# Optimization experiments

Measured on AMD Instinct MI355X. Metric: run time of the kernel, lower is better.

The kernel has to match this reference:

```python
import jax, jax.numpy as jnp
import numpy as np

D = 512        # embed_dim
H = 2048       # expert hidden (4*D)
E = 8          # num_experts
TOPK = 2       # num_experts_per_tok


def setup_inputs() -> dict:
    key = jax.random.key(0)
    ks = jax.random.split(key, 5)
    s = 0.02
    x = jax.random.normal(ks[0], (4, 8192, D), dtype=jnp.float32)
    gate_w = jax.random.normal(ks[1], (D, E), dtype=jnp.float32) * s
    W1 = jax.random.normal(ks[2], (E, D, H), dtype=jnp.float32) * s
    W3 = jax.random.normal(ks[3], (E, D, H), dtype=jnp.float32) * s
    W2 = jax.random.normal(ks[4], (E, H, D), dtype=jnp.float32) * s
    return {"x": x, "gate_w": gate_w, "W1": W1, "W2": W2, "W3": W3}


def reference(x, gate_w, W1, W2, W3):
    B, S, _ = x.shape
    xt = x.reshape(-1, D)                      # [T, D]
    T = xt.shape[0]
    gate_logits = xt @ gate_w                  # [T, E]
    w, idx = jax.lax.top_k(gate_logits, TOPK)  # [T, k]
    w = jax.nn.softmax(w, axis=1).astype(xt.dtype)
    # combine weights: comb[t, e] = routing weight of expert e for token t (0 if unselected)
    comb = jnp.zeros((T, E), dtype=xt.dtype).at[jnp.arange(T)[:, None], idx].add(w)
    out = jnp.zeros_like(xt)
    for e in range(E):
        h = jax.nn.silu(xt @ W1[e]) * (xt @ W3[e])   # [T, H]
        out = out + (h @ W2[e]) * comb[:, e:e + 1]
    return out.reshape(B, S, D)
```

## Files before the change

kernel.cpp:

```cpp
#include <hip/hip_runtime.h>
#include <stdint.h>

#define D_DIM 512
#define H_DIM 2048
#define E_NUM 8
#define TOPK_N 2

typedef __attribute__((ext_vector_type(8))) short bf16x8;
typedef __attribute__((ext_vector_type(4))) float f32x4;

#define GLOAD_LDS16(gsrc, ldst)                                                     \
    __builtin_amdgcn_global_load_lds(                                               \
        (const __attribute__((address_space(1))) void*)(gsrc),                      \
        (__attribute__((address_space(3))) void*)(ldst), 16, 0, 0)

static __device__ __forceinline__ unsigned short f2bf(float f) {
    unsigned u = __float_as_uint(f);
    unsigned r = (u + 0x7fffu + ((u >> 16) & 1u)) >> 16;
    return (unsigned short)r;
}

__global__ void init_kernel(int* list_token, float* list_w, unsigned short* zrow, int cap) {
    int id = blockIdx.x * blockDim.x + threadIdx.x;
    if (id < cap) { list_token[id] = -1; list_w[id] = 0.f; }
    if (id < D_DIM) zrow[id] = 0;
}

__global__ void gwt_kernel(const float* __restrict__ gw, float* __restrict__ gwT) {
    int id = blockIdx.x * blockDim.x + threadIdx.x;
    int e = id >> 9, d = id & 511;
    gwT[id] = gw[d * E_NUM + e];
}

__global__ void gate_cvt_kernel(const float* __restrict__ x, const float* __restrict__ gwT,
                                unsigned short* __restrict__ xb,
                                int* __restrict__ ridx, float* __restrict__ rw, int T) {
    int wave = threadIdx.x >> 6;
    int lane = threadIdx.x & 63;
    int t = blockIdx.x * 4 + wave;
    if (t >= T) return;
    const float* xr = x + (size_t)t * D_DIM + lane * 8;
    float4 a = *(const float4*)xr;
    float4 b = *(const float4*)(xr + 4);
    union { unsigned short s[8]; uint4 v; } o;
    o.s[0] = f2bf(a.x); o.s[1] = f2bf(a.y); o.s[2] = f2bf(a.z); o.s[3] = f2bf(a.w);
    o.s[4] = f2bf(b.x); o.s[5] = f2bf(b.y); o.s[6] = f2bf(b.z); o.s[7] = f2bf(b.w);
    *(uint4*)(xb + (size_t)t * D_DIM + lane * 8) = o.v;
    float acc[8];
#pragma unroll
    for (int e = 0; e < 8; ++e) {
        const float* g = gwT + e * D_DIM + lane * 8;
        float4 g0 = *(const float4*)g;
        float4 g1 = *(const float4*)(g + 4);
        acc[e] = a.x * g0.x + a.y * g0.y + a.z * g0.z + a.w * g0.w
               + b.x * g1.x + b.y * g1.y + b.z * g1.z + b.w * g1.w;
    }
#pragma unroll
    for (int off = 32; off > 0; off >>= 1) {
#pragma unroll
        for (int e = 0; e < 8; ++e) acc[e] += __shfl_xor(acc[e], off, 64);
    }
    if (lane == 0) {
        int e0 = 0; float l0 = acc[0];
#pragma unroll
        for (int e = 1; e < 8; ++e) if (acc[e] > l0) { l0 = acc[e]; e0 = e; }
        int e1 = -1; float l1 = -1e30f;
#pragma unroll
        for (int e = 0; e < 8; ++e) if (e != e0 && acc[e] > l1) { l1 = acc[e]; e1 = e; }
        float w0 = 1.f / (1.f + expf(l1 - l0));
        ridx[t * 2] = e0; ridx[t * 2 + 1] = e1;
        rw[t * 2] = w0;  rw[t * 2 + 1] = 1.f - w0;
    }
}

__global__ void tconv_kernel(const float* __restrict__ in, unsigned short* __restrict__ out,
                             int R, int C) {
    __shared__ float tile[32][33];
    int e = blockIdx.z;
    const float* src = in + (size_t)e * R * C;
    unsigned short* dst = out + (size_t)e * R * C;
    int c = blockIdx.x * 32 + threadIdx.x;
#pragma unroll
    for (int i = 0; i < 4; ++i) {
        int r = blockIdx.y * 32 + threadIdx.y + i * 8;
        tile[threadIdx.y + i * 8][threadIdx.x] = src[(size_t)r * C + c];
    }
    __syncthreads();
    int r2 = blockIdx.y * 32 + threadIdx.x;
#pragma unroll
    for (int i = 0; i < 4; ++i) {
        int c2 = blockIdx.x * 32 + threadIdx.y + i * 8;
        dst[(size_t)c2 * R + r2] = f2bf(tile[threadIdx.x][threadIdx.y + i * 8]);
    }
}

__global__ void hist_kernel(const int* __restrict__ ridx, int* __restrict__ partial, int npairs) {
    __shared__ int cnt[E_NUM];
    if (threadIdx.x < E_NUM) cnt[threadIdx.x] = 0;
    __syncthreads();
    for (int i = blockIdx.x * blockDim.x + threadIdx.x; i < npairs; i += gridDim.x * blockDim.x)
        atomicAdd(&cnt[ridx[i]], 1);
    __syncthreads();
    if (threadIdx.x < E_NUM) partial[blockIdx.x * E_NUM + threadIdx.x] = cnt[threadIdx.x];
}

__global__ void scan_kernel(const int* __restrict__ partial, int* __restrict__ seg,
                            int* __restrict__ block_base) {
    __shared__ int sp[64 * E_NUM];
    __shared__ int segl[E_NUM + 1];
    int tid = threadIdx.x;
    if (tid < 64 * E_NUM) sp[tid] = partial[tid];
    __syncthreads();
    if (tid == 0) {
        int off = 0;
        for (int e = 0; e < E_NUM; ++e) {
            segl[e] = off;
            int c = 0;
            for (int b = 0; b < 64; ++b) c += sp[b * E_NUM + e];
            off += (c + 127) & ~127;
        }
        segl[E_NUM] = off;
    }
    __syncthreads();
    if (tid < E_NUM) {
        int run = segl[tid];
        for (int b = 0; b < 64; ++b) { block_base[b * E_NUM + tid] = run; run += sp[b * E_NUM + tid]; }
        seg[tid] = segl[tid];
        if (tid == 0) seg[E_NUM] = segl[E_NUM];
    }
}

__global__ void scatter_kernel(const int* __restrict__ ridx, const float* __restrict__ rw,
                               const int* __restrict__ block_base,
                               int* __restrict__ list_token, float* __restrict__ list_w, int npairs) {
    __shared__ int base[E_NUM];
    __shared__ int cnt[E_NUM];
    if (threadIdx.x < E_NUM) { base[threadIdx.x] = block_base[blockIdx.x * E_NUM + threadIdx.x]; cnt[threadIdx.x] = 0; }
    __syncthreads();
    for (int i = blockIdx.x * blockDim.x + threadIdx.x; i < npairs; i += gridDim.x * blockDim.x) {
        int e = ridx[i];
        int pos = base[e] + atomicAdd(&cnt[e], 1);
        list_token[pos] = i >> 1;
        list_w[pos] = rw[i];
    }
}

__global__ __launch_bounds__(256) void gemm1_kernel(
    const unsigned short* __restrict__ xb,
    const unsigned short* __restrict__ w1t,
    const unsigned short* __restrict__ w3t,
    const unsigned short* __restrict__ zrow,
    const int* __restrict__ list_token,
    const int* __restrict__ seg,
    unsigned short* __restrict__ hbuf,
    int chunk_base, int MT, int MG) {
    __shared__ short As[2][128 * 64];
    __shared__ short Bs[2][128 * 64];

    int bfl = blockIdx.x;
    int xcd = bfl & 7;
    int idx = bfl >> 3;
    int mlocal = idx % MG;
    int yt = idx / MG;
    int mt = mlocal * 8 + xcd;
    if (mt >= MT) return;

    int tid = threadIdx.x;
    int w = tid >> 6, l = tid & 63;
    int m0 = mt * 128;
    int slot0 = chunk_base + m0;
    int n0 = yt * 64;

    int e = 0;
#pragma unroll
    for (int i = 0; i < E_NUM - 1; ++i) if (slot0 >= seg[i + 1]) e = i + 1;
    const unsigned short* b1 = w1t + ((size_t)e * H_DIM + n0) * D_DIM;
    const unsigned short* b3 = w3t + ((size_t)e * H_DIM + n0) * D_DIM;

    int lr8 = l >> 3, p = l & 7;
    const unsigned short* aptr[4];
    const unsigned short* bptr[4];
#pragma unroll
    for (int q = 0; q < 4; ++q) {
        int row = (q * 4 + w) * 8 + lr8;
        int c = p ^ (row & 7);
        int tok = list_token[slot0 + row];
        aptr[q] = (tok >= 0 ? xb + (size_t)tok * D_DIM : zrow) + c * 8;
        bptr[q] = (row < 64 ? b1 + (size_t)row * D_DIM
                            : b3 + (size_t)(row - 64) * D_DIM) + c * 8;
    }

    int wm = (w & 1) * 64;
    int wn = (w >> 1) * 32;
    int lrr = l & 15;
    int lk = (l >> 4) * 8;

    f32x4 acc1[4][2] = {};
    f32x4 acc3[4][2] = {};

#define G1_STAGE(K0, BUF)                                                           \
    {                                                                               \
        _Pragma("unroll")                                                           \
        for (int q = 0; q < 4; ++q) {                                               \
            GLOAD_LDS16(aptr[q] + (K0), &As[BUF][(q * 4 + w) * 512]);               \
            GLOAD_LDS16(bptr[q] + (K0), &Bs[BUF][(q * 4 + w) * 512]);               \
        }                                                                           \
    }

#define G1_COMPUTE(BUF)                                                             \
    {                                                                               \
        _Pragma("unroll")                                                           \
        for (int ks = 0; ks < 64; ks += 32) {                                       \
            int cblk = (ks + lk) >> 3;                                              \
            bf16x8 af[4], b1f[2], b3f[2];                                           \
            _Pragma("unroll")                                                       \
            for (int i = 0; i < 4; ++i) {                                           \
                int row = wm + i * 16 + lrr;                                        \
                af[i] = *(const bf16x8*)&As[BUF][row * 64 + ((cblk ^ (row & 7)) << 3)]; \
            }                                                                       \
            _Pragma("unroll")                                                       \
            for (int j = 0; j < 2; ++j) {                                           \
                int r1 = wn + j * 16 + lrr;                                         \
                b1f[j] = *(const bf16x8*)&Bs[BUF][r1 * 64 + ((cblk ^ (r1 & 7)) << 3)]; \
                int r3 = 64 + wn + j * 16 + lrr;                                    \
                b3f[j] = *(const bf16x8*)&Bs[BUF][r3 * 64 + ((cblk ^ (r3 & 7)) << 3)]; \
            }                                                                       \
            __builtin_amdgcn_s_setprio(1);                                          \
            _Pragma("unroll")                                                       \
            for (int i = 0; i < 4; ++i)                                             \
                _Pragma("unroll")                                                   \
                for (int j = 0; j < 2; ++j) {                                       \
                    acc1[i][j] = __builtin_amdgcn_mfma_f32_16x16x32_bf16(af[i], b1f[j], acc1[i][j], 0, 0, 0); \
                    acc3[i][j] = __builtin_amdgcn_mfma_f32_16x16x32_bf16(af[i], b3f[j], acc3[i][j], 0, 0, 0); \
                }                                                                   \
            __builtin_amdgcn_s_setprio(0);                                          \
        }                                                                           \
    }

    G1_STAGE(0, 0);
    __syncthreads();
#pragma unroll
    for (int t = 0; t < 8; t += 2) {
        G1_STAGE((t + 1) * 64, 1);
        G1_COMPUTE(0);
        __syncthreads();
        if (t + 2 < 8) G1_STAGE((t + 2) * 64, 0);
        G1_COMPUTE(1);
        __syncthreads();
    }
#undef G1_STAGE
#undef G1_COMPUTE

    int lrow0 = (l >> 4) * 4, lcol = l & 15;
#pragma unroll
    for (int i = 0; i < 4; ++i)
#pragma unroll
        for (int j = 0; j < 2; ++j)
#pragma unroll
            for (int r = 0; r < 4; ++r) {
                int row = wm + i * 16 + lrow0 + r;
                int col = wn + j * 16 + lcol;
                float v1 = acc1[i][j][r];
                float v3 = acc3[i][j][r];
                float h = v1 / (1.f + __expf(-v1)) * v3;
                hbuf[(size_t)(m0 + row) * H_DIM + n0 + col] = f2bf(h);
            }
}

__global__ __launch_bounds__(256) void gemm2_kernel(
    const unsigned short* __restrict__ hbuf,
    const unsigned short* __restrict__ w2t,
    const int* __restrict__ list_token,
    const float* __restrict__ list_w,
    const int* __restrict__ seg,
    float* __restrict__ out,
    int chunk_base, int MT) {
    __shared__ short As[2][128 * 64];
    __shared__ short Bs[2][128 * 64];

    int bfl = blockIdx.x;
    int xcd = bfl & 7;
    int idx = bfl >> 3;
    int yt = idx & 3;
    int mlocal = idx >> 2;
    int mt = mlocal * 8 + xcd;
    if (mt >= MT) return;

    int tid = threadIdx.x;
    int w = tid >> 6, l = tid & 63;
    int m0 = mt * 128;
    int slot0 = chunk_base + m0;
    int n0 = yt * 128;

    int e = 0;
#pragma unroll
    for (int i = 0; i < E_NUM - 1; ++i) if (slot0 >= seg[i + 1]) e = i + 1;
    const unsigned short* b2 = w2t + ((size_t)e * D_DIM + n0) * H_DIM;

    int lr8 = l >> 3, p = l & 7;
    const unsigned short* aptr[4];
    const unsigned short* bptr[4];
#pragma unroll
    for (int q = 0; q < 4; ++q) {
        int row = (q * 4 + w) * 8 + lr8;
        int c = p ^ (row & 7);
        aptr[q] = hbuf + (size_t)(m0 + row) * H_DIM + c * 8;
        bptr[q] = b2 + (size_t)row * H_DIM + c * 8;
    }

    int wm = (w & 1) * 64;
    int wn = (w >> 1) * 64;
    int lrr = l & 15;
    int lk = (l >> 4) * 8;

    f32x4 acc[4][4] = {};

#define G2_STAGE(K0, BUF)                                                           \
    {                                                                               \
        _Pragma("unroll")                                                           \
        for (int q = 0; q < 4; ++q) {                                               \
            GLOAD_LDS16(aptr[q] + (K0), &As[BUF][(q * 4 + w) * 512]);               \
            GLOAD_LDS16(bptr[q] + (K0), &Bs[BUF][(q * 4 + w) * 512]);               \
        }                                                                           \
    }

#define G2_COMPUTE(BUF)                                                             \
    {                                                                               \
        _Pragma("unroll")                                                           \
        for (int ks = 0; ks < 64; ks += 32) {                                       \
            int cblk = (ks + lk) >> 3;                                              \
            bf16x8 af[4], bf[4];                                                    \
            _Pragma("unroll")                                                       \
            for (int i = 0; i < 4; ++i) {                                           \
                int row = wm + i * 16 + lrr;                                        \
                af[i] = *(const bf16x8*)&As[BUF][row * 64 + ((cblk ^ (row & 7)) << 3)]; \
            }                                                                       \
            _Pragma("unroll")                                                       \
            for (int j = 0; j < 4; ++j) {                                           \
                int row = wn + j * 16 + lrr;                                        \
                bf[j] = *(const bf16x8*)&Bs[BUF][row * 64 + ((cblk ^ (row & 7)) << 3)]; \
            }                                                                       \
            __builtin_amdgcn_s_setprio(1);                                          \
            _Pragma("unroll")                                                       \
            for (int i = 0; i < 4; ++i)                                             \
                _Pragma("unroll")                                                   \
                for (int j = 0; j < 4; ++j)                                         \
                    acc[i][j] = __builtin_amdgcn_mfma_f32_16x16x32_bf16(af[i], bf[j], acc[i][j], 0, 0, 0); \
            __builtin_amdgcn_s_setprio(0);                                          \
        }                                                                           \
    }

    G2_STAGE(0, 0);
    __syncthreads();
    for (int t = 0; t < 32; t += 2) {
        G2_STAGE((t + 1) * 64, 1);
        G2_COMPUTE(0);
        __syncthreads();
        if (t + 2 < 32) G2_STAGE((t + 2) * 64, 0);
        G2_COMPUTE(1);
        __syncthreads();
    }
#undef G2_STAGE
#undef G2_COMPUTE

    int lrow0 = (l >> 4) * 4, lcol = l & 15;
#pragma unroll
    for (int i = 0; i < 4; ++i)
#pragma unroll
        for (int r = 0; r < 4; ++r) {
            int row = wm + i * 16 + lrow0 + r;
            int tok = list_token[slot0 + row];
            if (tok < 0) continue;
            float wgt = list_w[slot0 + row];
#pragma unroll
            for (int j = 0; j < 4; ++j) {
                int col = wn + j * 16 + lcol;
                atomicAdd(&out[(size_t)tok * D_DIM + n0 + col], acc[i][j][r] * wgt);
            }
        }
}

extern "C" void kernel_launch(void* const* d_in, const int* in_sizes, int n_in,
                              void* d_out, int out_size, void* d_ws, size_t ws_size,
                              hipStream_t stream) {
    const float* x  = (const float*)d_in[0];
    const float* gw = (const float*)d_in[1];
    const float* W1 = (const float*)d_in[2];
    const float* W2 = (const float*)d_in[3];
    const float* W3 = (const float*)d_in[4];
    float* out = (float*)d_out;

    int T = in_sizes[0] / D_DIM;
    int npairs = T * TOPK_N;
    const int CAP = npairs + E_NUM * 128;

    char* p = (char*)d_ws;
    size_t off = 0;
    auto take = [&](size_t bytes) {
        char* r = p + off;
        off = (off + bytes + 255) & ~(size_t)255;
        return r;
    };
    int* seg           = (int*)take((E_NUM + 1) * 4);
    int* partial       = (int*)take(64 * E_NUM * 4);
    int* block_base    = (int*)take(64 * E_NUM * 4);
    int* list_token    = (int*)take((size_t)CAP * 4);
    float* list_w      = (float*)take((size_t)CAP * 4);
    int* ridx          = (int*)take((size_t)npairs * 4);
    float* rw          = (float*)take((size_t)npairs * 4);
    float* gwT         = (float*)take((size_t)E_NUM * D_DIM * 4);
    unsigned short* zrow = (unsigned short*)take((size_t)D_DIM * 2);
    unsigned short* xb  = (unsigned short*)take((size_t)T * D_DIM * 2);
    unsigned short* w1t = (unsigned short*)take((size_t)E_NUM * D_DIM * H_DIM * 2);
    unsigned short* w3t = (unsigned short*)take((size_t)E_NUM * D_DIM * H_DIM * 2);
    unsigned short* w2t = (unsigned short*)take((size_t)E_NUM * D_DIM * H_DIM * 2);

    size_t hbuf2_bytes = (size_t)(CAP / 2) * H_DIM * 2;
    int NCHUNK = (ws_size >= off + hbuf2_bytes + 4096) ? 2 : 4;
    int chunk_slots = CAP / NCHUNK;
    int MT = chunk_slots / 128;
    int MG = (MT + 7) / 8;
    unsigned short* hbuf = (unsigned short*)take((size_t)chunk_slots * H_DIM * 2);

    hipMemsetAsync(d_out, 0, (size_t)out_size * sizeof(float), stream);

    init_kernel<<<(CAP + 255) / 256, 256, 0, stream>>>(list_token, list_w, zrow, CAP);
    gwt_kernel<<<(E_NUM * D_DIM) / 256, 256, 0, stream>>>(gw, gwT);

    gate_cvt_kernel<<<T / 4, 256, 0, stream>>>(x, gwT, xb, ridx, rw, T);

    dim3 tb(32, 8);
    tconv_kernel<<<dim3(H_DIM / 32, D_DIM / 32, E_NUM), tb, 0, stream>>>(W1, w1t, D_DIM, H_DIM);
    tconv_kernel<<<dim3(H_DIM / 32, D_DIM / 32, E_NUM), tb, 0, stream>>>(W3, w3t, D_DIM, H_DIM);
    tconv_kernel<<<dim3(D_DIM / 32, H_DIM / 32, E_NUM), tb, 0, stream>>>(W2, w2t, H_DIM, D_DIM);

    hist_kernel<<<64, 256, 0, stream>>>(ridx, partial, npairs);
    scan_kernel<<<1, 512, 0, stream>>>(partial, seg, block_base);
    scatter_kernel<<<64, 256, 0, stream>>>(ridx, rw, block_base, list_token, list_w, npairs);

    int g1_grid = 8 * MG * (H_DIM / 64);
    int g2_grid = 8 * MG * (D_DIM / 128);
    for (int c = 0; c < NCHUNK; ++c) {
        int cb = c * chunk_slots;
        gemm1_kernel<<<g1_grid, 256, 0, stream>>>(
            xb, w1t, w3t, zrow, list_token, seg, hbuf, cb, MT, MG);
        gemm2_kernel<<<g2_grid, 256, 0, stream>>>(
            hbuf, w2t, list_token, list_w, seg, out, cb, MT);
    }
}
```

Measured before the change: 917.0 us.

## Deepen GEMM prefetch with vmcnt waits and force four hidden-buffer chunks

```diff
diff --git a/kernel.cpp b/kernel.cpp
--- a/kernel.cpp
+++ b/kernel.cpp
@@ -13,6 +13,10 @@
     __builtin_amdgcn_global_load_lds(                                               \
         (const __attribute__((address_space(1))) void*)(gsrc),                      \
         (__attribute__((address_space(3))) void*)(ldst), 16, 0, 0)
+
+#define WAITVM(N) asm volatile("s_waitcnt vmcnt(" #N ")" ::: "memory")
+#define SCB() __builtin_amdgcn_sched_barrier(0)
+#define BAR() __builtin_amdgcn_s_barrier()
 
 static __device__ __forceinline__ unsigned short f2bf(float f) {
     unsigned u = __float_as_uint(f);
@@ -238,15 +242,23 @@
     }
 
     G1_STAGE(0, 0);
-    __syncthreads();
+    G1_STAGE(64, 1);
 #pragma unroll
     for (int t = 0; t < 8; t += 2) {
-        G1_STAGE((t + 1) * 64, 1);
+        WAITVM(8);
+        BAR();
+        SCB();
         G1_COMPUTE(0);
-        __syncthreads();
+        SCB();
+        BAR();
         if (t + 2 < 8) G1_STAGE((t + 2) * 64, 0);
+        if (t < 6) { WAITVM(8); } else { WAITVM(0); }
+        BAR();
+        SCB();
         G1_COMPUTE(1);
-        __syncthreads();
+        SCB();
+        BAR();
+        if (t + 3 < 8) G1_STAGE((t + 3) * 64, 1);
     }
 #undef G1_STAGE
 #undef G1_COMPUTE
@@ -351,15 +363,35 @@
     }
 
     G2_STAGE(0, 0);
-    __syncthreads();
-    for (int t = 0; t < 32; t += 2) {
-        G2_STAGE((t + 1) * 64, 1);
+    G2_STAGE(64, 1);
+    for (int t = 0; t < 30; t += 2) {
+        WAITVM(8);
+        BAR();
+        SCB();
         G2_COMPUTE(0);
-        __syncthreads();
-        if (t + 2 < 32) G2_STAGE((t + 2) * 64, 0);
+        SCB();
+        BAR();
+        G2_STAGE((t + 2) * 64, 0);
+        WAITVM(8);
+        BAR();
+        SCB();
         G2_COMPUTE(1);
-        __syncthreads();
-    }
+        SCB();
+        BAR();
+        G2_STAGE((t + 3) * 64, 1);
+    }
+    WAITVM(8);
+    BAR();
+    SCB();
+    G2_COMPUTE(0);
+    SCB();
+    BAR();
+    WAITVM(0);
+    BAR();
+    SCB();
+    G2_COMPUTE(1);
+    SCB();
+    BAR();
 #undef G2_STAGE
 #undef G2_COMPUTE
 
@@ -393,6 +425,10 @@
     int T = in_sizes[0] / D_DIM;
     int npairs = T * TOPK_N;
     const int CAP = npairs + E_NUM * 128;
+    const int NCHUNK = 4;
+    int chunk_slots = CAP / NCHUNK;
+    int MT = chunk_slots / 128;
+    int MG = (MT + 7) / 8;
 
     char* p = (char*)d_ws;
     size_t off = 0;
@@ -414,13 +450,8 @@
     unsigned short* w1t = (unsigned short*)take((size_t)E_NUM * D_DIM * H_DIM * 2);
     unsigned short* w3t = (unsigned short*)take((size_t)E_NUM * D_DIM * H_DIM * 2);
     unsigned short* w2t = (unsigned short*)take((size_t)E_NUM * D_DIM * H_DIM * 2);
-
-    size_t hbuf2_bytes = (size_t)(CAP / 2) * H_DIM * 2;
-    int NCHUNK = (ws_size >= off + hbuf2_bytes + 4096) ? 2 : 4;
-    int chunk_slots = CAP / NCHUNK;
-    int MT = chunk_slots / 128;
-    int MG = (MT + 7) / 8;
     unsigned short* hbuf = (unsigned short*)take((size_t)chunk_slots * H_DIM * 2);
+    (void)ws_size;
 
     hipMemsetAsync(d_out, 0, (size_t)out_size * sizeof(float), stream);
 
```

Measured after the change: 956.0 us. 1.04x slower.

## Use 4-stage K=32 LDS pipeline with vmcnt waits in both expert GEMMs

Applied to the files above, without the earlier changes.

```diff
diff --git a/kernel.cpp b/kernel.cpp
--- a/kernel.cpp
+++ b/kernel.cpp
@@ -13,6 +13,10 @@
     __builtin_amdgcn_global_load_lds(                                               \
         (const __attribute__((address_space(1))) void*)(gsrc),                      \
         (__attribute__((address_space(3))) void*)(ldst), 16, 0, 0)
+
+#define WAITVM(N) asm volatile("s_waitcnt vmcnt(" #N ")" ::: "memory")
+#define SCB() __builtin_amdgcn_sched_barrier(0)
+#define BAR() __builtin_amdgcn_s_barrier()
 
 static __device__ __forceinline__ unsigned short f2bf(float f) {
     unsigned u = __float_as_uint(f);
@@ -154,8 +158,8 @@
     const int* __restrict__ seg,
     unsigned short* __restrict__ hbuf,
     int chunk_base, int MT, int MG) {
-    __shared__ short As[2][128 * 64];
-    __shared__ short Bs[2][128 * 64];
+    __shared__ __align__(16) short As[4][4096];
+    __shared__ __align__(16) short Bs[4][4096];
 
     int bfl = blockIdx.x;
     int xcd = bfl & 7;
@@ -177,79 +181,95 @@
     const unsigned short* b1 = w1t + ((size_t)e * H_DIM + n0) * D_DIM;
     const unsigned short* b3 = w3t + ((size_t)e * H_DIM + n0) * D_DIM;
 
-    int lr8 = l >> 3, p = l & 7;
-    const unsigned short* aptr[4];
-    const unsigned short* bptr[4];
-#pragma unroll
-    for (int q = 0; q < 4; ++q) {
-        int row = (q * 4 + w) * 8 + lr8;
-        int c = p ^ (row & 7);
-        int tok = list_token[slot0 + row];
-        aptr[q] = (tok >= 0 ? xb + (size_t)tok * D_DIM : zrow) + c * 8;
-        bptr[q] = (row < 64 ? b1 + (size_t)row * D_DIM
-                            : b3 + (size_t)(row - 64) * D_DIM) + c * 8;
-    }
+    int seg0 = w, seg1 = 4 + w;
+    int r0 = seg0 * 16 + (l >> 2);
+    int r1 = seg1 * 16 + (l >> 2);
+    int gsrc8 = ((l & 3) ^ ((l >> 3) & 3)) * 8;
+    int tok0 = list_token[slot0 + r0];
+    int tok1 = list_token[slot0 + r1];
+    const unsigned short* pa0 = (tok0 >= 0 ? xb + (size_t)tok0 * D_DIM : zrow) + gsrc8;
+    const unsigned short* pa1 = (tok1 >= 0 ? xb + (size_t)tok1 * D_DIM : zrow) + gsrc8;
+    const unsigned short* pb0 = b1 + (size_t)r0 * D_DIM + gsrc8;
+    const unsigned short* pb1 = b3 + (size_t)(r1 - 64) * D_DIM + gsrc8;
 
     int wm = (w & 1) * 64;
     int wn = (w >> 1) * 32;
     int lrr = l & 15;
-    int lk = (l >> 4) * 8;
+    int gq = l >> 4;
+    int aoff[4], b1o[2], b3o[2];
+#pragma unroll
+    for (int i = 0; i < 4; ++i) {
+        int row = wm + i * 16 + lrr;
+        aoff[i] = row * 64 + ((gq ^ ((row >> 1) & 3)) << 4);
+    }
+#pragma unroll
+    for (int j = 0; j < 2; ++j) {
+        int rA = wn + j * 16 + lrr;
+        b1o[j] = rA * 64 + ((gq ^ ((rA >> 1) & 3)) << 4);
+        int rB = 64 + wn + j * 16 + lrr;
+        b3o[j] = rB * 64 + ((gq ^ ((rB >> 1) & 3)) << 4);
+    }
 
     f32x4 acc1[4][2] = {};
     f32x4 acc3[4][2] = {};
 
-#define G1_STAGE(K0, BUF)                                                           \
+#define G1_STAGE(KO, SBUF)                                                          \
     {                                                                               \
-        _Pragma("unroll")                                                           \
-        for (int q = 0; q < 4; ++q) {                                               \
-            GLOAD_LDS16(aptr[q] + (K0), &As[BUF][(q * 4 + w) * 512]);               \
-            GLOAD_LDS16(bptr[q] + (K0), &Bs[BUF][(q * 4 + w) * 512]);               \
-        }                                                                           \
+        GLOAD_LDS16(pa0 + (KO) * 32, &As[SBUF][seg0 * 512]);                        \
+        GLOAD_LDS16(pa1 + (KO) * 32, &As[SBUF][seg1 * 512]);                        \
+        GLOAD_LDS16(pb0 + (KO) * 32, &Bs[SBUF][seg0 * 512]);                        \
+        GLOAD_LDS16(pb1 + (KO) * 32, &Bs[SBUF][seg1 * 512]);                        \
     }
 
 #define G1_COMPUTE(BUF)                                                             \
     {                                                                               \
+        const char* Ab = (const char*)As[BUF];                                      \
+        const char* Bb = (const char*)Bs[BUF];                                      \
+        bf16x8 af[4], f1[2], f3[2];                                                 \
         _Pragma("unroll")                                                           \
-        for (int ks = 0; ks < 64; ks += 32) {                                       \
-            int cblk = (ks + lk) >> 3;                                              \
-            bf16x8 af[4], b1f[2], b3f[2];                                           \
-            _Pragma("unroll")                                                       \
-            for (int i = 0; i < 4; ++i) {                                           \
-                int row = wm + i * 16 + lrr;                                        \
-                af[i] = *(const bf16x8*)&As[BUF][row * 64 + ((cblk ^ (row & 7)) << 3)]; \
-            }                                                                       \
+        for (int i = 0; i < 4; ++i) af[i] = *(const bf16x8*)(Ab + aoff[i]);         \
+        _Pragma("unroll")                                                           \
+        for (int j = 0; j < 2; ++j) {                                               \
+            f1[j] = *(const bf16x8*)(Bb + b1o[j]);                                  \
+            f3[j] = *(const bf16x8*)(Bb + b3o[j]);                                  \
+        }                                                                           \
+        __builtin_amdgcn_s_setprio(1);                                              \
+        _Pragma("unroll")                                                           \
+        for (int i = 0; i < 4; ++i)                                                 \
             _Pragma("unroll")                                                       \
             for (int j = 0; j < 2; ++j) {                                           \
-                int r1 = wn + j * 16 + lrr;                                         \
-                b1f[j] = *(const bf16x8*)&Bs[BUF][r1 * 64 + ((cblk ^ (r1 & 7)) << 3)]; \
-                int r3 = 64 + wn + j * 16 + lrr;                                    \
-                b3f[j] = *(const bf16x8*)&Bs[BUF][r3 * 64 + ((cblk ^ (r3 & 7)) << 3)]; \
+                acc1[i][j] = __builtin_amdgcn_mfma_f32_16x16x32_bf16(af[i], f1[j], acc1[i][j], 0, 0, 0); \
+                acc3[i][j] = __builtin_amdgcn_mfma_f32_16x16x32_bf16(af[i], f3[j], acc3[i][j], 0, 0, 0); \
             }                                                                       \
-            __builtin_amdgcn_s_setprio(1);                                          \
-            _Pragma("unroll")                                                       \
-            for (int i = 0; i < 4; ++i)                                             \
-                _Pragma("unroll")                                                   \
-                for (int j = 0; j < 2; ++j) {                                       \
-                    acc1[i][j] = __builtin_amdgcn_mfma_f32_16x16x32_bf16(af[i], b1f[j], acc1[i][j], 0, 0, 0); \
-                    acc3[i][j] = __builtin_amdgcn_mfma_f32_16x16x32_bf16(af[i], b3f[j], acc3[i][j], 0, 0, 0); \
-                }                                                                   \
-            __builtin_amdgcn_s_setprio(0);                                          \
-        }                                                                           \
-    }
+        __builtin_amdgcn_s_setprio(0);                                              \
+    }
+
+#define G1_STEP8S(T, CB, SB) { WAITVM(8); BAR(); SCB(); G1_STAGE((T) + 3, SB); G1_COMPUTE(CB); }
+#define G1_STEP8(CB)  { WAITVM(8); BAR(); SCB(); G1_COMPUTE(CB); }
+#define G1_STEP4(CB)  { WAITVM(4); BAR(); SCB(); G1_COMPUTE(CB); }
+#define G1_STEP0(CB)  { WAITVM(0); BAR(); SCB(); G1_COMPUTE(CB); }
 
     G1_STAGE(0, 0);
-    __syncthreads();
-#pragma unroll
-    for (int t = 0; t < 8; t += 2) {
-        G1_STAGE((t + 1) * 64, 1);
-        G1_COMPUTE(0);
-        __syncthreads();
-        if (t + 2 < 8) G1_STAGE((t + 2) * 64, 0);
-        G1_COMPUTE(1);
-        __syncthreads();
-    }
+    G1_STAGE(1, 1);
+    G1_STAGE(2, 2);
+#pragma unroll
+    for (int t = 0; t < 12; t += 4) {
+        G1_STEP8S(t + 0, 0, 3);
+        G1_STEP8S(t + 1, 1, 0);
+        G1_STEP8S(t + 2, 2, 1);
+        G1_STEP8S(t + 3, 3, 2);
+    }
+    G1_STEP8S(12, 0, 3);
+    G1_STEP8(1);
+    G1_STEP4(2);
+    G1_STEP0(3);
+
 #undef G1_STAGE
 #undef G1_COMPUTE
+#undef G1_STEP8S
+#undef G1_STEP8
+#undef G1_STEP4
+#undef G1_STEP0
 
     int lrow0 = (l >> 4) * 4, lcol = l & 15;
 #pragma unroll
@@ -275,8 +295,8 @@
     const int* __restrict__ seg,
     float* __restrict__ out,
     int chunk_base, int MT) {
-    __shared__ short As[2][128 * 64];
-    __shared__ short Bs[2][128 * 64];
+    __shared__ __align__(16) short As[4][4096];
+    __shared__ __align__(16) short Bs[4][4096];
 
     int bfl = blockIdx.x;
     int xcd = bfl & 7;
@@ -297,71 +317,82 @@
     for (int i = 0; i < E_NUM - 1; ++i) if (slot0 >= seg[i + 1]) e = i + 1;
     const unsigned short* b2 = w2t + ((size_t)e * D_DIM + n0) * H_DIM;
 
-    int lr8 = l >> 3, p = l & 7;
-    const unsigned short* aptr[4];
-    const unsigned short* bptr[4];
-#pragma unroll
-    for (int q = 0; q < 4; ++q) {
-        int row = (q * 4 + w) * 8 + lr8;
-        int c = p ^ (row & 7);
-        aptr[q] = hbuf + (size_t)(m0 + row) * H_DIM + c * 8;
-        bptr[q] = b2 + (size_t)row * H_DIM + c * 8;
-    }
+    int seg0 = w, seg1 = 4 + w;
+    int r0 = seg0 * 16 + (l >> 2);
+    int r1 = seg1 * 16 + (l >> 2);
+    int gsrc8 = ((l & 3) ^ ((l >> 3) & 3)) * 8;
+    const unsigned short* pa0 = hbuf + (size_t)(m0 + r0) * H_DIM + gsrc8;
+    const unsigned short* pa1 = hbuf + (size_t)(m0 + r1) * H_DIM + gsrc8;
+    const unsigned short* pb0 = b2 + (size_t)r0 * H_DIM + gsrc8;
+    const unsigned short* pb1 = b2 + (size_t)r1 * H_DIM + gsrc8;
 
     int wm = (w & 1) * 64;
     int wn = (w >> 1) * 64;
     int lrr = l & 15;
-    int lk = (l >> 4) * 8;
+    int gq = l >> 4;
+    int aoff[4], boff[4];
+#pragma unroll
+    for (int i = 0; i < 4; ++i) {
+        int rowA = wm + i * 16 + lrr;
+        aoff[i] = rowA * 64 + ((gq ^ ((rowA >> 1) & 3)) << 4);
+        int rowB = wn + i * 16 + lrr;
+        boff[i] = rowB * 64 + ((gq ^ ((rowB >> 1) & 3)) << 4);
+    }
 
     f32x4 acc[4][4] = {};
 
-#define G2_STAGE(K0, BUF)                                                           \
+#define G2_STAGE(KO, SBUF)                                                          \
     {                                                                               \
-        _Pragma("unroll")                                                           \
-        for (int q = 0; q < 4; ++q) {                                               \
-            GLOAD_LDS16(aptr[q] + (K0), &As[BUF][(q * 4 + w) * 512]);               \
-            GLOAD_LDS16(bptr[q] + (K0), &Bs[BUF][(q * 4 + w) * 512]);               \
-        }                                                                           \
+        GLOAD_LDS16(pa0 + (KO) * 32, &As[SBUF][seg0 * 512]);                        \
+        GLOAD_LDS16(pa1 + (KO) * 32, &As[SBUF][seg1 * 512]);                        \
+        GLOAD_LDS16(pb0 + (KO) * 32, &Bs[SBUF][seg0 * 512]);                        \
+        GLOAD_LDS16(pb1 + (KO) * 32, &Bs[SBUF][seg1 * 512]);                        \
     }
 
 #define G2_COMPUTE(BUF)                                                             \
     {                                                                               \
+        const char* Ab = (const char*)As[BUF];                                      \
+        const char* Bb = (const char*)Bs[BUF];                                      \
+        bf16x8 af[4], bf[4];                                                        \
         _Pragma("unroll")                                                           \
-        for (int ks = 0; ks < 64; ks += 32) {                                       \
-            int cblk = (ks + lk) >> 3;                                              \
-            bf16x8 af[4], bf[4];                                                    \
+        for (int i = 0; i < 4; ++i) {                                               \
+            af[i] = *(const bf16x8*)(Ab + aoff[i]);                                 \
+            bf[i] = *(const bf16x8*)(Bb + boff[i]);                                 \
+        }                                                                           \
+        __builtin_amdgcn_s_setprio(1);                                              \
+        _Pragma("unroll")                                                           \
+        for (int i = 0; i < 4; ++i)                                                 \
             _Pragma("unroll")                                                       \
-            for (int i = 0; i < 4; ++i) {                                           \
-                int row = wm + i * 16 + lrr;                                        \
-                af[i] = *(const bf16x8*)&As[BUF][row * 64 + ((cblk ^ (row & 7)) << 3)]; \
-            }                                                                       \
-            _Pragma("unroll")                                                       \
-            for (int j = 0; j < 4; ++j) {                                           \
-                int row = wn + j * 16 + lrr;                                        \
-                bf[j] = *(const bf16x8*)&Bs[BUF][row * 64 + ((cblk ^ (row & 7)) << 3)]; \
-            }                                                                       \
-            __builtin_amdgcn_s_setprio(1);                                          \
-            _Pragma("unroll")                                                       \
-            for (int i = 0; i < 4; ++i)                                             \
-                _Pragma("unroll")                                                   \
-                for (int j = 0; j < 4; ++j)                                         \
-                    acc[i][j] = __builtin_amdgcn_mfma_f32_16x16x32_bf16(af[i], bf[j], acc[i][j], 0, 0, 0); \
-            __builtin_amdgcn_s_setprio(0);                                          \
-        }                                                                           \
-    }
+            for (int j = 0; j < 4; ++j)                                             \
+                acc[i][j] = __builtin_amdgcn_mfma_f32_16x16x32_bf16(af[i], bf[j], acc[i][j], 0, 0, 0); \
+        __builtin_amdgcn_s_setprio(0);                                              \
+    }
+
+#define G2_STEP8S(T, CB, SB) { WAITVM(8); BAR(); SCB(); G2_STAGE((T) + 3, SB); G2_COMPUTE(CB); }
+#define G2_STEP8(CB)  { WAITVM(8); BAR(); SCB(); G2_COMPUTE(CB); }
+#define G2_STEP4(CB)  { WAITVM(4); BAR(); SCB(); G2_COMPUTE(CB); }
+#define G2_STEP0(CB)  { WAITVM(0); BAR(); SCB(); G2_COMPUTE(CB); }
 
     G2_STAGE(0, 0);
-    __syncthreads();
-    for (int t = 0; t < 32; t += 2) {
-        G2_STAGE((t + 1) * 64, 1);
-        G2_COMPUTE(0);
-        __syncthreads();
-        if (t + 2 < 32) G2_STAGE((t + 2) * 64, 0);
-        G2_COMPUTE(1);
-        __syncthreads();
-    }
+    G2_STAGE(1, 1);
+    G2_STAGE(2, 2);
+    for (int t = 0; t < 60; t += 4) {
+        G2_STEP8S(t + 0, 0, 3);
+        G2_STEP8S(t + 1, 1, 0);
+        G2_STEP8S(t + 2, 2, 1);
+        G2_STEP8S(t + 3, 3, 2);
+    }
+    G2_STEP8S(60, 0, 3);
+    G2_STEP8(1);
+    G2_STEP4(2);
+    G2_STEP0(3);
+
 #undef G2_STAGE
 #undef G2_COMPUTE
+#undef G2_STEP8S
+#undef G2_STEP8
+#undef G2_STEP4
+#undef G2_STEP0
 
     int lrow0 = (l >> 4) * 4, lcol = l & 15;
 #pragma unroll
@@ -393,6 +424,10 @@
     int T = in_sizes[0] / D_DIM;
     int npairs = T * TOPK_N;
     const int CAP = npairs + E_NUM * 128;
+    const int NCHUNK = 4;
+    int chunk_slots = CAP / NCHUNK;
+    int MT = chunk_slots / 128;
+    int MG = (MT + 7) / 8;
 
     char* p = (char*)d_ws;
     size_t off = 0;
@@ -414,13 +449,8 @@
     unsigned short* w1t = (unsigned short*)take((size_t)E_NUM * D_DIM * H_DIM * 2);
     unsigned short* w3t = (unsigned short*)take((size_t)E_NUM * D_DIM * H_DIM * 2);
     unsigned short* w2t = (unsigned short*)take((size_t)E_NUM * D_DIM * H_DIM * 2);
-
-    size_t hbuf2_bytes = (size_t)(CAP / 2) * H_DIM * 2;
-    int NCHUNK = (ws_size >= off + hbuf2_bytes + 4096) ? 2 : 4;
-    int chunk_slots = CAP / NCHUNK;
-    int MT = chunk_slots / 128;
-    int MG = (MT + 7) / 8;
     unsigned short* hbuf = (unsigned short*)take((size_t)chunk_slots * H_DIM * 2);
+    (void)ws_size;
 
     hipMemsetAsync(d_out, 0, (size_t)out_size * sizeof(float), stream);
 
```

Measured after the change: 1.025 ms. 1.12x slower.
